# Kernel tuning notes

Hardware: AMD Instinct MI355X
Metric: run time of the kernel (lower is better)

Reference implementation:

```python
import jax, jax.numpy as jnp
import numpy as np

NUM_HEADS = 4
LN_EPS = 1e-5


def setup_inputs() -> dict:
    key = jax.random.key(0)
    B, S, D = 4, 2048, 1024
    H = NUM_HEADS
    hd = D // H
    ks = jax.random.split(key, 8)
    s = 1.0 / np.sqrt(hd)
    inp = {
        "embeddings": jax.random.normal(ks[0], (B, S, D), dtype=jnp.float32),
        # per-head Q/K/V projection weights (torch Linear weight layout [out,in])
        "Wq": jax.random.normal(ks[1], (H, hd, hd), dtype=jnp.float32) * s,
        "Wk": jax.random.normal(ks[2], (H, hd, hd), dtype=jnp.float32) * s,
        "Wv": jax.random.normal(ks[3], (H, hd, hd), dtype=jnp.float32) * s,
        # lens bias scalars: causal, intent, temporal, normative (init values from module)
        "bias_scalars": jnp.array([0.1, 0.15, 0.05, 0.2], dtype=jnp.float32),
        "Wo_w": jax.random.normal(ks[4], (D, D), dtype=jnp.float32) / np.sqrt(D),
        "Wo_b": jnp.zeros((D,), dtype=jnp.float32),
        "ln_g": jnp.ones((D,), dtype=jnp.float32),
        "ln_b": jnp.zeros((D,), dtype=jnp.float32),
    }
    return inp


def _legal_biases(x, bias_scalars):
    """x: [B,H,S,hd] per-head embeddings. Returns stacked bias [B,H,S,S]."""
    B, H, S, hd = x.shape
    # head 0: CAUSAL -> strictly upper triangular mask * causal_bias
    causal = jnp.triu(jnp.ones((S, S), dtype=x.dtype), k=1)  # [S,S]
    b0 = causal[None] * bias_scalars[0]                      # [1,S,S] -> bcast B
    b0 = jnp.broadcast_to(b0, (B, S, S))
    # head 1: INTENTIONALITY -> outer product of embedding norms, global-mean threshold
    mag1 = jnp.linalg.norm(x[:, 1], axis=-1)                 # [B,S]
    intent = mag1[:, :, None] * mag1[:, None, :]             # [B,S,S]
    b1 = (intent > intent.mean()).astype(x.dtype) * bias_scalars[1]
    # head 2: TEMPORAL -> exp(-|i-j|/S)
    pos = jnp.arange(S, dtype=x.dtype)
    prox = jnp.exp(-jnp.abs(pos[:, None] - pos[None, :]) / S)  # [S,S]
    b2 = jnp.broadcast_to(prox[None] * bias_scalars[2], (B, S, S))
    # head 3: NORMATIVE -> outer product of last feature, > 0.5 threshold
    v3 = x[:, 3, :, -1]                                      # [B,S]
    viol = v3[:, :, None] * v3[:, None, :]                   # [B,S,S]
    b3 = (viol > 0.5).astype(x.dtype) * bias_scalars[3]
    return jnp.stack([b0, b1, b2, b3], axis=1)               # [B,H,S,S]


def _forward(embeddings, Wq, Wk, Wv, bias_scalars, Wo_w, Wo_b, ln_g, ln_b):
    B, S, D = embeddings.shape
    H = NUM_HEADS
    hd = D // H
    x = embeddings.reshape(B, S, H, hd).transpose(0, 2, 1, 3)     # [B,H,S,hd]
    # torch Linear: y = x @ W.T
    Q = jnp.einsum('bhsd,hed->bhse', x, Wq)
    K = jnp.einsum('bhsd,hed->bhse', x, Wk)
    V = jnp.einsum('bhsd,hed->bhse', x, Wv)
    scores = jnp.einsum('bhse,bhte->bhst', Q, K) / np.sqrt(hd)    # [B,H,S,S]
    scores = scores + _legal_biases(x, bias_scalars)
    weights = jax.nn.softmax(scores, axis=-1)                     # [B,H,S,S]
    attended = jnp.einsum('bhst,bhte->bhse', weights, V)          # [B,H,S,hd]
    concat = attended.transpose(0, 2, 1, 3).reshape(B, S, D)      # head order = concat order
    out = concat @ Wo_w.T + Wo_b
    # layer_norm(out + embeddings)
    y = out + embeddings
    mu = y.mean(axis=-1, keepdims=True)
    var = ((y - mu) ** 2).mean(axis=-1, keepdims=True)
    output = (y - mu) / jnp.sqrt(var + LN_EPS) * ln_g + ln_b      # [B,S,D]
    average_weights = weights.mean(axis=1)                        # [B,S,S]
    guilt = jax.nn.softmax(average_weights.sum(axis=-1), axis=-1) # [B,S]
    return output, average_weights, guilt


def reference(embeddings, Wq, Wk, Wv, bias_scalars, Wo_w, Wo_b, ln_g, ln_b):
    return _forward(embeddings, Wq, Wk, Wv, bias_scalars, Wo_w, Wo_b, ln_g, ln_b)
```

## Files before the change

### kernel.cpp

```cpp
#include <hip/hip_runtime.h>
#include <hip/hip_bf16.h>
#include <math.h>

#define S_ 2048
#define D_ 1024
#define H_ 4
#define HD_ 256
#define B_ 4

typedef __hip_bfloat16 bf16;
typedef short s16x8 __attribute__((ext_vector_type(8)));
typedef float f32x4 __attribute__((ext_vector_type(4)));

#define GLOAD16(g, l)                                             \
    __builtin_amdgcn_global_load_lds(                             \
        (const __attribute__((address_space(1))) void*)(g),       \
        (__attribute__((address_space(3))) void*)(l), 16, 0, 0)


template <int MODE>
__global__ __launch_bounds__(256) void mfma_nt(
    int K,
    const bf16* __restrict__ A, int lda, long sA_b, long sA_h,
    const bf16* __restrict__ Bm, int ldb, long sB_b, long sB_h,
    void* __restrict__ Cp, int ldc, long sC_b, long sC_h,
    int zdiv, int bbase,
    const double* __restrict__ mag1d, const double* __restrict__ v3d,
    const double* __restrict__ meand, const float* __restrict__ bias_sc)
{
    __shared__ __align__(16) short As[128 * 32];
    __shared__ __align__(16) short Bs[128 * 32];

    const int tid = threadIdx.x;
    const int w = tid >> 6, lane = tid & 63;
    const int srow = lane >> 2;
    const int scol = (((lane & 3) ^ (srow & 3)) << 3);
    const int quad = lane >> 4, r = lane & 15;
    const int qx = quad ^ (r & 3);
    const int wr = (w >> 1) * 64, wc = (w & 1) * 64;
    const int zb = blockIdx.z / zdiv, zh = blockIdx.z % zdiv;

    const bf16* Ap = A + (size_t)zb * sA_b + (size_t)zh * sA_h +
                     (size_t)blockIdx.y * 128 * lda;
    const bf16* Bp = Bm + (size_t)zb * sB_b + (size_t)zh * sB_h +
                     (size_t)blockIdx.x * 128 * ldb;

    f32x4 acc[4][4] = {};

    for (int k0 = 0; k0 < K; k0 += 32) {
        if (k0) __syncthreads();
#pragma unroll
        for (int l = 0; l < 2; l++) {
            GLOAD16(Ap + (size_t)(w * 32 + l * 16 + srow) * lda + (k0 + scol),
                    &As[(w * 32 + l * 16) * 32]);
            GLOAD16(Bp + (size_t)(w * 32 + l * 16 + srow) * ldb + (k0 + scol),
                    &Bs[(w * 32 + l * 16) * 32]);
        }
        __syncthreads();

        s16x8 af[4], bfv[4];
        const s16x8* A8 = (const s16x8*)As;
        const s16x8* B8 = (const s16x8*)Bs;
#pragma unroll
        for (int i = 0; i < 4; i++) af[i] = A8[(wr + i * 16 + r) * 4 + qx];
#pragma unroll
        for (int j = 0; j < 4; j++) bfv[j] = B8[(wc + j * 16 + r) * 4 + qx];
#pragma unroll
        for (int i = 0; i < 4; i++)
#pragma unroll
            for (int j = 0; j < 4; j++)
                acc[i][j] = __builtin_amdgcn_mfma_f32_16x16x32_bf16(
                    af[i], bfv[j], acc[i][j], 0, 0, 0);
    }

    const int row0 = blockIdx.y * 128 + wr + quad * 4;
    const int col0 = blockIdx.x * 128 + wc + r;

    if (MODE == 0) {
        float* C = (float*)Cp + (size_t)zb * sC_b + (size_t)zh * sC_h;
#pragma unroll
        for (int i = 0; i < 4; i++)
#pragma unroll
            for (int j = 0; j < 4; j++)
#pragma unroll
                for (int p = 0; p < 4; p++)
                    C[(size_t)(row0 + i * 16 + p) * ldc + (col0 + j * 16)] = acc[i][j][p];
    } else if (MODE == 1) {
        bf16* C = (bf16*)Cp + (size_t)zb * sC_b + (size_t)zh * sC_h;
#pragma unroll
        for (int i = 0; i < 4; i++)
#pragma unroll
            for (int j = 0; j < 4; j++)
#pragma unroll
                for (int p = 0; p < 4; p++)
                    C[(size_t)(row0 + i * 16 + p) * ldc + (col0 + j * 16)] =
                        __float2bfloat16(acc[i][j][p]);
    } else {
        float* C = (float*)Cp + (size_t)zb * sC_b + (size_t)zh * sC_h;
        const int h = zh;
        const int bbatch = bbase + zb;
        const float bsc = bias_sc[h];
        if (h == 0) {
#pragma unroll
            for (int i = 0; i < 4; i++)
#pragma unroll
                for (int j = 0; j < 4; j++)
#pragma unroll
                    for (int p = 0; p < 4; p++) {
                        const int rr = row0 + i * 16 + p, c = col0 + j * 16;
                        C[(size_t)rr * ldc + c] = acc[i][j][p] + ((c > rr) ? bsc : 0.0f);
                    }
        } else if (h == 2) {
#pragma unroll
            for (int i = 0; i < 4; i++)
#pragma unroll
                for (int j = 0; j < 4; j++)
#pragma unroll
                    for (int p = 0; p < 4; p++) {
                        const int rr = row0 + i * 16 + p, c = col0 + j * 16;
                        int d = c - rr; d = d < 0 ? -d : d;
                        C[(size_t)rr * ldc + c] =
                            acc[i][j][p] + bsc * expf(-(float)d * (1.0f / 2048.0f));
                    }
        } else {
            const double* src = (h == 1) ? mag1d : v3d;
            const double thr = (h == 1) ? meand[0] : 0.5;
            double rv[16], cv[4];
#pragma unroll
            for (int i = 0; i < 4; i++)
#pragma unroll
                for (int p = 0; p < 4; p++)
                    rv[i * 4 + p] = src[(size_t)bbatch * S_ + row0 + i * 16 + p];
#pragma unroll
            for (int j = 0; j < 4; j++)
                cv[j] = src[(size_t)bbatch * S_ + col0 + j * 16];
#pragma unroll
            for (int i = 0; i < 4; i++)
#pragma unroll
                for (int j = 0; j < 4; j++)
#pragma unroll
                    for (int p = 0; p < 4; p++) {
                        const int rr = row0 + i * 16 + p, c = col0 + j * 16;
                        C[(size_t)rr * ldc + c] =
                            acc[i][j][p] + ((rv[i * 4 + p] * cv[j] > thr) ? bsc : 0.0f);
                    }
        }
    }
}

__global__ __launch_bounds__(512) void mfma_pv(const bf16* __restrict__ Pm,
                                               const bf16* __restrict__ Vt,
                                               bf16* __restrict__ Cc) {
    __shared__ __align__(16) short L[6][12288];

    const int tid = threadIdx.x;
    const int w = tid >> 6, lane = tid & 63;
    const int quad = lane >> 4, r = lane & 15;
    const int qx = quad ^ (r & 3);
    const int wr = (w >> 2) * 64, wc = (w & 3) * 64;

    const int bid = blockIdx.x;
    const int bh = (bid & 7) * 2 + ((bid >> 3) >> 4);
    const int rb = (bid >> 3) & 15;
    const int b = bh >> 2, h = bh & 3;

    const bf16* Ap = Pm + ((size_t)bh * S_ + (size_t)rb * 128) * S_;
    const bf16* Bp = Vt + (size_t)(h * B_ + b) * HD_ * S_;

    const int srow = tid >> 2;
    const int scol = (((tid & 3) ^ (srow & 3)) << 3);
    const int wbase = w * 512;

    f32x4 acc[4][4] = {};

    auto stage = [&](int bs, int t) {
        short* sb = &L[bs][0];
        const int k0 = t * 32;
        GLOAD16(Ap + (size_t)srow * S_ + (k0 + scol), sb + wbase);
        GLOAD16(Bp + (size_t)srow * S_ + (k0 + scol), sb + 4096 + wbase);
        GLOAD16(Bp + (size_t)(128 + srow) * S_ + (k0 + scol), sb + 8192 + wbase);
    };
    auto compute = [&](int bs) {
        const s16x8* A8 = (const s16x8*)&L[bs][0];
        const s16x8* B8 = (const s16x8*)&L[bs][4096];
        s16x8 af[4], bfv[4];
#pragma unroll
        for (int i = 0; i < 4; i++) af[i] = A8[(wr + i * 16 + r) * 4 + qx];
#pragma unroll
        for (int j = 0; j < 4; j++) bfv[j] = B8[(wc + j * 16 + r) * 4 + qx];
        __builtin_amdgcn_s_setprio(1);
#pragma unroll
        for (int i = 0; i < 4; i++)
#pragma unroll
            for (int j = 0; j < 4; j++)
                acc[i][j] = __builtin_amdgcn_mfma_f32_16x16x32_bf16(
                    af[i], bfv[j], acc[i][j], 0, 0, 0);
        __builtin_amdgcn_s_setprio(0);
    };

#define PV_WAITB(N)                                           \
    asm volatile("s_waitcnt vmcnt(" #N ")" ::: "memory");     \
    __builtin_amdgcn_s_barrier();                             \
    __builtin_amdgcn_sched_barrier(0);

    stage(0, 0); stage(1, 1); stage(2, 2); stage(3, 3); stage(4, 4);

    int cb = 0, sn = 5;
#pragma unroll 1
    for (int t = 0; t < 59; ++t) {
        PV_WAITB(12);
        stage(sn, t + 5);
        compute(cb);
        cb = (cb == 5) ? 0 : cb + 1;
        sn = (sn == 5) ? 0 : sn + 1;
    }
    PV_WAITB(12); compute(cb); cb = (cb == 5) ? 0 : cb + 1;
    PV_WAITB(9);  compute(cb); cb = (cb == 5) ? 0 : cb + 1;
    PV_WAITB(6);  compute(cb); cb = (cb == 5) ? 0 : cb + 1;
    PV_WAITB(3);  compute(cb); cb = (cb == 5) ? 0 : cb + 1;
    PV_WAITB(0);  compute(cb);
#undef PV_WAITB

    const int row0 = rb * 128 + wr + quad * 4;
    const int col0 = h * HD_ + wc + r;
    bf16* C = Cc + (size_t)b * S_ * D_;
#pragma unroll
    for (int i = 0; i < 4; i++)
#pragma unroll
        for (int j = 0; j < 4; j++)
#pragma unroll
            for (int p = 0; p < 4; p++)
                C[(size_t)(row0 + i * 16 + p) * D_ + col0 + j * 16] =
                    __float2bfloat16(acc[i][j][p]);
}

__global__ __launch_bounds__(256) void cvt_bf16(const float* __restrict__ in,
                                                bf16* __restrict__ out, int n,
                                                float scale) {
    const size_t i0 = ((size_t)blockIdx.x * 256 + threadIdx.x) * 4;
    if (i0 + 3 < (size_t)n) {
        const float4 v = *(const float4*)(in + i0);
        out[i0 + 0] = __float2bfloat16(v.x * scale);
        out[i0 + 1] = __float2bfloat16(v.y * scale);
        out[i0 + 2] = __float2bfloat16(v.z * scale);
        out[i0 + 3] = __float2bfloat16(v.w * scale);
    }
}

__global__ __launch_bounds__(256) void transpose_v(const bf16* __restrict__ in,
                                                   bf16* __restrict__ out) {
    const int h = blockIdx.z / B_, b = blockIdx.z % B_;
    const int e0 = blockIdx.x * 64, s0 = blockIdx.y * 64;
    __shared__ short t[64][66];
    const int tid = threadIdx.x;
    const int rr = tid >> 2;
    const int cc = (tid & 3) << 4;
    const bf16* ip = in + (((size_t)h * B_ * S_) + (size_t)b * S_ + s0) * HD_ + e0;
    const s16x8 v0 = *(const s16x8*)(ip + (size_t)rr * HD_ + cc);
    const s16x8 v1 = *(const s16x8*)(ip + (size_t)rr * HD_ + cc + 8);
#pragma unroll
    for (int i = 0; i < 8; i++) {
        t[rr][cc + i] = v0[i];
        t[rr][cc + 8 + i] = v1[i];
    }
    __syncthreads();
    bf16* op = out + (((size_t)h * B_ + b) * HD_ + e0 + rr) * S_ + s0 + cc;
    s16x8 o0, o1;
#pragma unroll
    for (int i = 0; i < 8; i++) {
        o0[i] = t[cc + i][rr];
        o1[i] = t[cc + 8 + i][rr];
    }
    *(s16x8*)op = o0;
    *(s16x8*)(op + 8) = o1;
}

__global__ __launch_bounds__(256) void prep_kernel(const float* __restrict__ emb,
                                                   double* __restrict__ mag1d,
                                                   double* __restrict__ v3d) {
    const long row = blockIdx.x;
    const int tid = threadIdx.x;
    const float x = emb[row * D_ + 256 + tid];
    __shared__ double red[256];
    red[tid] = (double)x * (double)x;
    __syncthreads();
    for (int off = 128; off > 0; off >>= 1) {
        if (tid < off) red[tid] += red[tid + off];
        __syncthreads();
    }
    if (tid == 0) {
        mag1d[row] = sqrt(red[0]);
        v3d[row] = (double)emb[row * D_ + 1023];
    }
}

__global__ __launch_bounds__(256) void mean_kernel(const double* __restrict__ mag1d,
                                                   double* __restrict__ meand) {
    const int tid = threadIdx.x;
    __shared__ double red[256];
    double acc = 0.0;
    for (int b = 0; b < B_; b++) {
        double ss = 0.0;
        for (int i = tid; i < S_; i += 256) ss += mag1d[(long)b * S_ + i];
        __syncthreads();
        red[tid] = ss;
        __syncthreads();
        for (int off = 128; off > 0; off >>= 1) {
            if (tid < off) red[tid] += red[tid + off];
            __syncthreads();
        }
        if (tid == 0) {
            const double rb = red[0] / (double)S_;
            acc += rb * rb;
        }
        __syncthreads();
    }
    if (tid == 0) meand[0] = acc / (double)B_;
}

__global__ __launch_bounds__(256) void softmax_fused(
    const float* __restrict__ scores, bf16* __restrict__ P, long p_h, int p_row,
    float* __restrict__ avgw, float* __restrict__ rowsum) {
    const int s = blockIdx.x, tid = threadIdx.x;
    __shared__ float red[256];
    float wacc[8] = {0, 0, 0, 0, 0, 0, 0, 0};
    for (int h = 0; h < H_; h++) {
        const float* rp = scores + ((size_t)h * S_ + s) * S_;
        bf16* pp = P + (size_t)h * p_h + (size_t)s * p_row;
        float v[8];
        float m = -1e30f;
#pragma unroll
        for (int i = 0; i < 8; i++) {
            v[i] = rp[tid + 256 * i];
            m = fmaxf(m, v[i]);
        }
        red[tid] = m;
        __syncthreads();
        for (int off = 128; off > 0; off >>= 1) {
            if (tid < off) red[tid] = fmaxf(red[tid], red[tid + off]);
            __syncthreads();
        }
        m = red[0];
        __syncthreads();
        float sum = 0.0f;
#pragma unroll
        for (int i = 0; i < 8; i++) {
            v[i] = expf(v[i] - m);
            sum += v[i];
        }
        red[tid] = sum;
        __syncthreads();
        for (int off = 128; off > 0; off >>= 1) {
            if (tid < off) red[tid] += red[tid + off];
            __syncthreads();
        }
        const float inv = 1.0f / red[0];
        __syncthreads();
#pragma unroll
        for (int i = 0; i < 8; i++) {
            const float wv = v[i] * inv;
            pp[tid + 256 * i] = __float2bfloat16(wv);
            wacc[i] += wv;
        }
    }
    float asum = 0.0f;
#pragma unroll
    for (int i = 0; i < 8; i++) {
        const float a = wacc[i] * 0.25f;
        avgw[(size_t)s * S_ + tid + 256 * i] = a;
        asum += a;
    }
    red[tid] = asum;
    __syncthreads();
    for (int off = 128; off > 0; off >>= 1) {
        if (tid < off) red[tid] += red[tid + off];
        __syncthreads();
    }
    if (tid == 0) rowsum[s] = red[0];
}

__global__ __launch_bounds__(256) void ln_kernel(float* __restrict__ out,
                                                 const float* __restrict__ emb,
                                                 const float* __restrict__ wob,
                                                 const float* __restrict__ g,
                                                 const float* __restrict__ beta) {
    const long row = blockIdx.x;
    float* o = out + row * D_;
    const float* e = emb + row * D_;
    const int tid = threadIdx.x;
    __shared__ float red[256];
    float v[4];
    float sum = 0.0f;
#pragma unroll
    for (int i = 0; i < 4; i++) {
        const int c = tid + 256 * i;
        v[i] = o[c] + wob[c] + e[c];
        sum += v[i];
    }
    red[tid] = sum;
    __syncthreads();
    for (int off = 128; off > 0; off >>= 1) {
        if (tid < off) red[tid] += red[tid + off];
        __syncthreads();
    }
    const float mu = red[0] * (1.0f / 1024.0f);
    __syncthreads();
    float vs = 0.0f;
#pragma unroll
    for (int i = 0; i < 4; i++) {
        const float d = v[i] - mu;
        vs += d * d;
    }
    red[tid] = vs;
    __syncthreads();
    for (int off = 128; off > 0; off >>= 1) {
        if (tid < off) red[tid] += red[tid + off];
        __syncthreads();
    }
    const float var = red[0] * (1.0f / 1024.0f);
    const float inv = 1.0f / sqrtf(var + 1e-5f);
#pragma unroll
    for (int i = 0; i < 4; i++) {
        const int c = tid + 256 * i;
        o[c] = (v[i] - mu) * inv * g[c] + beta[c];
    }
}

__global__ __launch_bounds__(256) void guilt_kernel(const float* __restrict__ rowsum,
                                                    float* __restrict__ guilt) {
    const int b = blockIdx.x, tid = threadIdx.x;
    const float* r = rowsum + (long)b * S_;
    float* gq = guilt + (long)b * S_;
    __shared__ float red[256];
    float v[8];
    float m = -1e30f;
#pragma unroll
    for (int i = 0; i < 8; i++) {
        v[i] = r[tid + 256 * i];
        m = fmaxf(m, v[i]);
    }
    red[tid] = m;
    __syncthreads();
    for (int off = 128; off > 0; off >>= 1) {
        if (tid < off) red[tid] = fmaxf(red[tid], red[tid + off]);
        __syncthreads();
    }
    m = red[0];
    __syncthreads();
    float sum = 0.0f;
#pragma unroll
    for (int i = 0; i < 8; i++) {
        v[i] = expf(v[i] - m);
        sum += v[i];
    }
    red[tid] = sum;
    __syncthreads();
    for (int off = 128; off > 0; off >>= 1) {
        if (tid < off) red[tid] += red[tid + off];
        __syncthreads();
    }
    const float inv = 1.0f / red[0];
#pragma unroll
    for (int i = 0; i < 8; i++) gq[tid + 256 * i] = v[i] * inv;
}

extern "C" void kernel_launch(void* const* d_in, const int* in_sizes, int n_in,
                              void* d_out, int out_size, void* d_ws, size_t ws_size,
                              hipStream_t stream) {
    const float* emb = (const float*)d_in[0];
    const float* Wq = (const float*)d_in[1];
    const float* Wk = (const float*)d_in[2];
    const float* Wv = (const float*)d_in[3];
    const float* bias_sc = (const float*)d_in[4];
    const float* Wo_w = (const float*)d_in[5];
    const float* Wo_b = (const float*)d_in[6];
    const float* ln_g = (const float*)d_in[7];
    const float* ln_bt = (const float*)d_in[8];

    char* ws = (char*)d_ws;
    size_t off = 0;
    auto alloc = [&](size_t bytes) {
        size_t o = off;
        off = (off + bytes + 255) & ~(size_t)255;
        return o;
    };
    bf16* embb = (bf16*)(ws + alloc((size_t)B_ * S_ * D_ * 2));
    bf16* concat = embb;
    bf16* Qm = (bf16*)(ws + alloc((size_t)H_ * B_ * S_ * HD_ * 2));
    bf16* Km = (bf16*)(ws + alloc((size_t)H_ * B_ * S_ * HD_ * 2));
    bf16* Vtb = (bf16*)(ws + alloc((size_t)H_ * B_ * HD_ * S_ * 2));
    bf16* Wqb = (bf16*)(ws + alloc((size_t)H_ * HD_ * HD_ * 2));
    bf16* Wkb = (bf16*)(ws + alloc((size_t)H_ * HD_ * HD_ * 2));
    bf16* Wvb = (bf16*)(ws + alloc((size_t)H_ * HD_ * HD_ * 2));
    bf16* Wob = (bf16*)(ws + alloc((size_t)D_ * D_ * 2));
    double* mag1d = (double*)(ws + alloc((size_t)B_ * S_ * 8));
    double* v3d = (double*)(ws + alloc((size_t)B_ * S_ * 8));
    double* meand = (double*)(ws + alloc(256));
    float* rowsum = (float*)(ws + alloc((size_t)B_ * S_ * 4));
    float* scores = (float*)(ws + alloc((size_t)H_ * S_ * S_ * 4));
    bf16* Vraw = (bf16*)scores;
    bf16* P = (bf16*)(ws + off);
    const size_t need_batched = off + (size_t)B_ * H_ * S_ * S_ * 2;
    const bool batched = ws_size >= need_batched;

    float* outp = (float*)d_out;
    float* avgw = outp + (size_t)B_ * S_ * D_;
    float* guilt = avgw + (size_t)B_ * S_ * S_;

    cvt_bf16<<<(B_ * S_ * D_) / 1024, 256, 0, stream>>>(emb, embb, B_ * S_ * D_, 1.0f);
    cvt_bf16<<<(H_ * HD_ * HD_) / 1024, 256, 0, stream>>>(Wq, Wqb, H_ * HD_ * HD_, 0.0625f);
    cvt_bf16<<<(H_ * HD_ * HD_) / 1024, 256, 0, stream>>>(Wk, Wkb, H_ * HD_ * HD_, 1.0f);
    cvt_bf16<<<(H_ * HD_ * HD_) / 1024, 256, 0, stream>>>(Wv, Wvb, H_ * HD_ * HD_, 1.0f);
    cvt_bf16<<<(D_ * D_) / 1024, 256, 0, stream>>>(Wo_w, Wob, D_ * D_, 1.0f);

    prep_kernel<<<B_ * S_, 256, 0, stream>>>(emb, mag1d, v3d);
    mean_kernel<<<1, 256, 0, stream>>>(mag1d, meand);

    {
        const dim3 g(HD_ / 128, (B_ * S_) / 128, H_);
        const long sQ = (long)B_ * S_ * HD_;
        mfma_nt<1><<<g, 256, 0, stream>>>(HD_, embb, D_, 0, HD_,
                                          Wqb, HD_, 0, (long)HD_ * HD_,
                                          Qm, HD_, 0, sQ, H_, 0,
                                          nullptr, nullptr, nullptr, nullptr);
        mfma_nt<1><<<g, 256, 0, stream>>>(HD_, embb, D_, 0, HD_,
                                          Wkb, HD_, 0, (long)HD_ * HD_,
                                          Km, HD_, 0, sQ, H_, 0,
                                          nullptr, nullptr, nullptr, nullptr);
        mfma_nt<1><<<g, 256, 0, stream>>>(HD_, embb, D_, 0, HD_,
                                          Wvb, HD_, 0, (long)HD_ * HD_,
                                          Vraw, HD_, 0, sQ, H_, 0,
                                          nullptr, nullptr, nullptr, nullptr);
    }
    transpose_v<<<dim3(HD_ / 64, S_ / 64, H_ * B_), 256, 0, stream>>>(Vraw, Vtb);

    for (int b = 0; b < B_; b++) {
        mfma_nt<3><<<dim3(S_ / 128, S_ / 128, H_), 256, 0, stream>>>(
            HD_,
            Qm + (size_t)b * S_ * HD_, HD_, 0, (long)B_ * S_ * HD_,
            Km + (size_t)b * S_ * HD_, HD_, 0, (long)B_ * S_ * HD_,
            scores, S_, 0, (long)S_ * S_,
            H_, b, mag1d, v3d, meand, bias_sc);
        if (batched) {
            softmax_fused<<<S_, 256, 0, stream>>>(
                scores, P + (size_t)b * H_ * S_ * S_, (long)S_ * S_, S_,
                avgw + (size_t)b * S_ * S_, rowsum + (size_t)b * S_);
        } else {
            softmax_fused<<<S_, 256, 0, stream>>>(
                scores, (bf16*)scores, 2L * S_ * S_, 2 * S_,
                avgw + (size_t)b * S_ * S_, rowsum + (size_t)b * S_);
            mfma_nt<1><<<dim3(HD_ / 128, S_ / 128, H_), 256, 0, stream>>>(
                S_,
                (const bf16*)scores, 2 * S_, 0, 2L * S_ * S_,
                Vtb + (size_t)b * HD_ * S_, S_, 0, (long)B_ * HD_ * S_,
                concat + (size_t)b * S_ * D_, D_, 0, HD_,
                H_, 0, nullptr, nullptr, nullptr, nullptr);
        }
    }
    if (batched) {
        mfma_pv<<<256, 512, 0, stream>>>(P, Vtb, concat);
    }

    mfma_nt<0><<<dim3(D_ / 128, (B_ * S_) / 128, 1), 256, 0, stream>>>(
        D_, concat, D_, 0, 0, Wob, D_, 0, 0, outp, D_, 0, 0,
        1, 0, nullptr, nullptr, nullptr, nullptr);

    ln_kernel<<<B_ * S_, 256, 0, stream>>>(outp, emb, Wo_b, ln_g, ln_bt);
    guilt_kernel<<<B_, 256, 0, stream>>>(rowsum, guilt);
}
```

Before: 509.2 us.

## Load P operands directly to registers in PV GEMM; vectorize softmax and layernorm

The PV matmul kernel now loads the P (A) operand straight from global memory into registers with inline dwordx4 loads, double-buffered in two register sets. Only V still goes through LDS, and its ring shrinks from six stages to three. This cuts LDS traffic and shared-memory footprint, which may raise occupancy, but the direct loads are less coalesced and the pipeline is shallower. Separately, the softmax and layernorm kernels switch to float4 loads and stores and packed bf16 stores to reduce memory instruction count.

```diff
diff --git a/kernel.cpp b/kernel.cpp
--- a/kernel.cpp
+++ b/kernel.cpp
@@ -10,6 +10,7 @@
 
 typedef __hip_bfloat16 bf16;
 typedef short s16x8 __attribute__((ext_vector_type(8)));
+typedef short s16x4 __attribute__((ext_vector_type(4)));
 typedef float f32x4 __attribute__((ext_vector_type(4)));
 
 #define GLOAD16(g, l)                                             \
@@ -17,6 +18,16 @@
         (const __attribute__((address_space(1))) void*)(g),       \
         (__attribute__((address_space(3))) void*)(l), 16, 0, 0)
 
+#define PLOAD(dst, p)                                             \
+    asm volatile("global_load_dwordx4 %0, %1, off"                \
+                 : "=&v"(dst) : "v"(p) : "memory")
+
+static __device__ inline short bfb(float x) {
+    bf16 t = __float2bfloat16(x);
+    short s;
+    __builtin_memcpy(&s, &t, 2);
+    return s;
+}
 
 template <int MODE>
 __global__ __launch_bounds__(256) void mfma_nt(
@@ -151,7 +162,7 @@
 __global__ __launch_bounds__(512) void mfma_pv(const bf16* __restrict__ Pm,
                                                const bf16* __restrict__ Vt,
                                                bf16* __restrict__ Cc) {
-    __shared__ __align__(16) short L[6][12288];
+    __shared__ __align__(16) short Lv[3][8192];
 
     const int tid = threadIdx.x;
     const int w = tid >> 6, lane = tid & 63;
@@ -169,23 +180,25 @@
 
     const int srow = tid >> 2;
     const int scol = (((tid & 3) ^ (srow & 3)) << 3);
-    const int wbase = w * 512;
 
     f32x4 acc[4][4] = {};
 
-    auto stage = [&](int bs, int t) {
-        short* sb = &L[bs][0];
+    const bf16* q0 = Ap + (size_t)(wr + 0 * 16 + r) * S_ + quad * 8;
+    const bf16* q1 = Ap + (size_t)(wr + 1 * 16 + r) * S_ + quad * 8;
+    const bf16* q2 = Ap + (size_t)(wr + 2 * 16 + r) * S_ + quad * 8;
+    const bf16* q3 = Ap + (size_t)(wr + 3 * 16 + r) * S_ + quad * 8;
+
+    s16x8 paA[4], paB[4];
+
+    auto stageV = [&](int bs, int t) {
         const int k0 = t * 32;
-        GLOAD16(Ap + (size_t)srow * S_ + (k0 + scol), sb + wbase);
-        GLOAD16(Bp + (size_t)srow * S_ + (k0 + scol), sb + 4096 + wbase);
-        GLOAD16(Bp + (size_t)(128 + srow) * S_ + (k0 + scol), sb + 8192 + wbase);
+        GLOAD16(Bp + (size_t)srow * S_ + (k0 + scol), &Lv[bs][w * 512]);
+        GLOAD16(Bp + (size_t)(128 + srow) * S_ + (k0 + scol),
+                &Lv[bs][4096 + w * 512]);
     };
-    auto compute = [&](int bs) {
-        const s16x8* A8 = (const s16x8*)&L[bs][0];
-        const s16x8* B8 = (const s16x8*)&L[bs][4096];
-        s16x8 af[4], bfv[4];
-#pragma unroll
-        for (int i = 0; i < 4; i++) af[i] = A8[(wr + i * 16 + r) * 4 + qx];
+    auto compute = [&](int bs, const s16x8* pa) {
+        const s16x8* B8 = (const s16x8*)&Lv[bs][0];
+        s16x8 bfv[4];
 #pragma unroll
         for (int j = 0; j < 4; j++) bfv[j] = B8[(wc + j * 16 + r) * 4 + qx];
         __builtin_amdgcn_s_setprio(1);
@@ -194,7 +207,7 @@
 #pragma unroll
             for (int j = 0; j < 4; j++)
                 acc[i][j] = __builtin_amdgcn_mfma_f32_16x16x32_bf16(
-                    af[i], bfv[j], acc[i][j], 0, 0, 0);
+                    pa[i], bfv[j], acc[i][j], 0, 0, 0);
         __builtin_amdgcn_s_setprio(0);
     };
 
@@ -203,22 +216,40 @@
     __builtin_amdgcn_s_barrier();                             \
     __builtin_amdgcn_sched_barrier(0);
 
-    stage(0, 0); stage(1, 1); stage(2, 2); stage(3, 3); stage(4, 4);
-
-    int cb = 0, sn = 5;
+    stageV(0, 0);
+    PLOAD(paA[0], q0); PLOAD(paA[1], q1); PLOAD(paA[2], q2); PLOAD(paA[3], q3);
+    stageV(1, 1);
+    PLOAD(paB[0], q0 + 32); PLOAD(paB[1], q1 + 32);
+    PLOAD(paB[2], q2 + 32); PLOAD(paB[3], q3 + 32);
+    q0 += 64; q1 += 64; q2 += 64; q3 += 64;
+
+    int cb = 0;
 #pragma unroll 1
-    for (int t = 0; t < 59; ++t) {
-        PV_WAITB(12);
-        stage(sn, t + 5);
-        compute(cb);
-        cb = (cb == 5) ? 0 : cb + 1;
-        sn = (sn == 5) ? 0 : sn + 1;
-    }
-    PV_WAITB(12); compute(cb); cb = (cb == 5) ? 0 : cb + 1;
-    PV_WAITB(9);  compute(cb); cb = (cb == 5) ? 0 : cb + 1;
-    PV_WAITB(6);  compute(cb); cb = (cb == 5) ? 0 : cb + 1;
-    PV_WAITB(3);  compute(cb); cb = (cb == 5) ? 0 : cb + 1;
-    PV_WAITB(0);  compute(cb);
+    for (int t = 0; t < 62; t += 2) {
+        PV_WAITB(6);
+        {
+            int sb = cb + 2; if (sb >= 3) sb -= 3;
+            stageV(sb, t + 2);
+        }
+        compute(cb, paA);
+        PLOAD(paA[0], q0); PLOAD(paA[1], q1); PLOAD(paA[2], q2); PLOAD(paA[3], q3);
+        q0 += 32; q1 += 32; q2 += 32; q3 += 32;
+        cb = (cb == 2) ? 0 : cb + 1;
+        PV_WAITB(6);
+        {
+            int sb = cb + 2; if (sb >= 3) sb -= 3;
+            stageV(sb, t + 3);
+        }
+        compute(cb, paB);
+        PLOAD(paB[0], q0); PLOAD(paB[1], q1); PLOAD(paB[2], q2); PLOAD(paB[3], q3);
+        q0 += 32; q1 += 32; q2 += 32; q3 += 32;
+        cb = (cb == 2) ? 0 : cb + 1;
+    }
+    PV_WAITB(6);
+    compute(cb, paA);
+    cb = (cb == 2) ? 0 : cb + 1;
+    PV_WAITB(0);
+    compute(cb, paB);
 #undef PV_WAITB
 
     const int row0 = rb * 128 + wr + quad * 4;
@@ -327,13 +358,12 @@
     for (int h = 0; h < H_; h++) {
         const float* rp = scores + ((size_t)h * S_ + s) * S_;
         bf16* pp = P + (size_t)h * p_h + (size_t)s * p_row;
-        float v[8];
+        const float4 va = ((const float4*)rp)[tid];
+        const float4 vb = ((const float4*)rp)[256 + tid];
+        float v[8] = {va.x, va.y, va.z, va.w, vb.x, vb.y, vb.z, vb.w};
         float m = -1e30f;
 #pragma unroll
-        for (int i = 0; i < 8; i++) {
-            v[i] = rp[tid + 256 * i];
-            m = fmaxf(m, v[i]);
-        }
+        for (int i = 0; i < 8; i++) m = fmaxf(m, v[i]);
         red[tid] = m;
         __syncthreads();
         for (int off = 128; off > 0; off >>= 1) {
@@ -356,20 +386,28 @@
         }
         const float inv = 1.0f / red[0];
         __syncthreads();
-#pragma unroll
-        for (int i = 0; i < 8; i++) {
-            const float wv = v[i] * inv;
-            pp[tid + 256 * i] = __float2bfloat16(wv);
-            wacc[i] += wv;
-        }
-    }
-    float asum = 0.0f;
-#pragma unroll
-    for (int i = 0; i < 8; i++) {
-        const float a = wacc[i] * 0.25f;
-        avgw[(size_t)s * S_ + tid + 256 * i] = a;
-        asum += a;
-    }
+        s16x4 pk0, pk1;
+#pragma unroll
+        for (int j = 0; j < 4; j++) {
+            const float w0 = v[j] * inv;
+            const float w1 = v[4 + j] * inv;
+            pk0[j] = bfb(w0);
+            pk1[j] = bfb(w1);
+            wacc[j] += w0;
+            wacc[4 + j] += w1;
+        }
+        *(s16x4*)(pp + (size_t)tid * 4) = pk0;
+        *(s16x4*)(pp + 1024 + (size_t)tid * 4) = pk1;
+    }
+    float4 a0, a1;
+    a0.x = wacc[0] * 0.25f; a0.y = wacc[1] * 0.25f;
+    a0.z = wacc[2] * 0.25f; a0.w = wacc[3] * 0.25f;
+    a1.x = wacc[4] * 0.25f; a1.y = wacc[5] * 0.25f;
+    a1.z = wacc[6] * 0.25f; a1.w = wacc[7] * 0.25f;
+    float* ar = avgw + (size_t)s * S_;
+    ((float4*)ar)[tid] = a0;
+    ((float4*)ar)[256 + tid] = a1;
+    const float asum = a0.x + a0.y + a0.z + a0.w + a1.x + a1.y + a1.z + a1.w;
     red[tid] = asum;
     __syncthreads();
     for (int off = 128; off > 0; off >>= 1) {
@@ -389,15 +427,12 @@
     const float* e = emb + row * D_;
     const int tid = threadIdx.x;
     __shared__ float red[256];
-    float v[4];
-    float sum = 0.0f;
-#pragma unroll
-    for (int i = 0; i < 4; i++) {
-        const int c = tid + 256 * i;
-        v[i] = o[c] + wob[c] + e[c];
-        sum += v[i];
-    }
-    red[tid] = sum;
+    const float4 vo = ((const float4*)o)[tid];
+    const float4 vw = ((const float4*)wob)[tid];
+    const float4 ve = ((const float4*)e)[tid];
+    float v[4] = {vo.x + vw.x + ve.x, vo.y + vw.y + ve.y,
+                  vo.z + vw.z + ve.z, vo.w + vw.w + ve.w};
+    red[tid] = v[0] + v[1] + v[2] + v[3];
     __syncthreads();
     for (int off = 128; off > 0; off >>= 1) {
         if (tid < off) red[tid] += red[tid + off];
@@ -419,11 +454,14 @@
     }
     const float var = red[0] * (1.0f / 1024.0f);
     const float inv = 1.0f / sqrtf(var + 1e-5f);
-#pragma unroll
-    for (int i = 0; i < 4; i++) {
-        const int c = tid + 256 * i;
-        o[c] = (v[i] - mu) * inv * g[c] + beta[c];
-    }
+    const float4 g4 = ((const float4*)g)[tid];
+    const float4 b4 = ((const float4*)beta)[tid];
+    float4 r4;
+    r4.x = (v[0] - mu) * inv * g4.x + b4.x;
+    r4.y = (v[1] - mu) * inv * g4.y + b4.y;
+    r4.z = (v[2] - mu) * inv * g4.z + b4.z;
+    r4.w = (v[3] - mu) * inv * g4.w + b4.w;
+    ((float4*)o)[tid] = r4;
 }
 
 __global__ __launch_bounds__(256) void guilt_kernel(const float* __restrict__ rowsum,
```

After: 536.7 us. 5.4% more time.
